# Optimization experiments

Measured on AMD Instinct MI355X. Metric: run time of the kernel, lower is better.

The kernel has to match this reference:

```python
import jax, jax.numpy as jnp
import numpy as np

B, N, E, H = 4, 4096, 1024, 16
D = E // H


def setup_inputs() -> dict:
    key = jax.random.key(0)
    ks = jax.random.split(key, 8)
    s = 1.0 / np.sqrt(E)
    x = jax.random.normal(ks[0], (B, N, E), dtype=jnp.float32)
    # binary multiplicative sparsity pattern over the head-head score matrix
    sparsity_pattern = jax.random.randint(ks[1], (H, H), 0, 2).astype(jnp.float32)
    Wq = jax.random.normal(ks[2], (E, E), dtype=jnp.float32) * s
    bq = jax.random.normal(ks[3], (E,), dtype=jnp.float32) * s
    Wk = jax.random.normal(ks[4], (E, E), dtype=jnp.float32) * s
    bk = jax.random.normal(ks[5], (E,), dtype=jnp.float32) * s
    Wv = jax.random.normal(ks[6], (E, E), dtype=jnp.float32) * s
    bv = jax.random.normal(ks[7], (E,), dtype=jnp.float32) * s
    return {"x": x, "sparsity_pattern": sparsity_pattern,
            "Wq": Wq, "bq": bq, "Wk": Wk, "bk": bk, "Wv": Wv, "bv": bv}


def reference(x, sparsity_pattern, Wq, bq, Wk, bk, Wv, bv):
    b, n, e = x.shape
    # torch Linear: y = x @ W.T + b
    q = (x @ Wq.T + bq).reshape(b, n, H, D)
    k = (x @ Wk.T + bk).reshape(b, n, H, D)
    v = (x @ Wv.T + bv).reshape(b, n, H, D)
    # torch.matmul over last two dims of [B,N,H,D]: scores are [B,N,H,H]
    scores = jnp.einsum('bnhd,bngd->bnhg', q, k) * sparsity_pattern
    attn = jax.nn.softmax(scores, axis=-1)
    out = jnp.einsum('bnhg,bngd->bnhd', attn, v).reshape(b, n, e)
    return out
```

## Files before the change

kernel.cpp:

```cpp
#include <hip/hip_runtime.h>
#include <hip/hip_bf16.h>

#define M_   16384
#define K_   1024
#define NQKV 3072

typedef _Float16 f16x4 __attribute__((ext_vector_type(4)));
typedef _Float16 f16x8 __attribute__((ext_vector_type(8)));
typedef float    f32x4 __attribute__((ext_vector_type(4)));

__global__ __launch_bounds__(256) void cvt_f32_f16(const float* __restrict__ in,
                                                   _Float16* __restrict__ o, int n4) {
  int i = blockIdx.x * blockDim.x + threadIdx.x;
  const int stride = gridDim.x * blockDim.x;
  for (; i < n4; i += stride) {
    float4 v = ((const float4*)in)[i];
    f16x4 h; h[0] = (_Float16)v.x; h[1] = (_Float16)v.y;
    h[2] = (_Float16)v.z; h[3] = (_Float16)v.w;
    *(f16x4*)&o[(size_t)i * 4] = h;
  }
}

__global__ __launch_bounds__(256) void cvt3_f32_f16(
    const float* __restrict__ a, const float* __restrict__ b,
    const float* __restrict__ c, _Float16* __restrict__ o, int n4each) {
  const float* src = (blockIdx.y == 0) ? a : (blockIdx.y == 1) ? b : c;
  _Float16* dst = o + (size_t)blockIdx.y * n4each * 4;
  int i = blockIdx.x * blockDim.x + threadIdx.x;
  const int stride = gridDim.x * blockDim.x;
  for (; i < n4each; i += stride) {
    float4 v = ((const float4*)src)[i];
    f16x4 h; h[0] = (_Float16)v.x; h[1] = (_Float16)v.y;
    h[2] = (_Float16)v.z; h[3] = (_Float16)v.w;
    *(f16x4*)&dst[(size_t)i * 4] = h;
  }
}

__global__ __launch_bounds__(512, 2) void gemm_qkv(
    const _Float16* __restrict__ xh, const _Float16* __restrict__ wh,
    const float* __restrict__ bq, const float* __restrict__ bk,
    const float* __restrict__ bv, _Float16* __restrict__ qkv)
{
  __shared__ __align__(16) _Float16 As[2][256 * 64];
  __shared__ __align__(16) _Float16 Bs[2][256 * 64];

  const int tid  = threadIdx.x;
  const int ln   = tid & 63;
  const int w    = tid >> 6;
  const int wm2  = w >> 2;
  const int wn4  = w & 3;
  const int lcol = ln & 15, quad = ln >> 4;

  const int bid = blockIdx.x;
  const int swz = (bid & 7) * 96 + (bid >> 3);
  const int m0 = (swz / 12) * 256;
  const int n0 = (swz % 12) * 256;

  f32x4 acc[8][4];
#pragma unroll
  for (int i = 0; i < 8; ++i)
#pragma unroll
    for (int j = 0; j < 4; ++j) acc[i][j] = f32x4{0.f, 0.f, 0.f, 0.f};

  f16x8 a0[4][2], a1[4][2], b0e[2][2], b0o[2][2], b1[2][2];

#define STAGE_A(BUF, KT, X)                                                    \
  { _Pragma("unroll")                                                          \
    for (int j = 0; j < 2; ++j) {                                              \
      const int c   = j * 512 + tid;                                           \
      const int rr  = c >> 3;                                                  \
      const int r   = (X) * 64 + (rr & 63) + ((rr >> 6) << 7);                 \
      const int cb  = (c & 7) ^ (r & 7);                                       \
      const int rr0 = j * 64 + w * 8;                                          \
      const int r0  = (X) * 64 + (rr0 & 63) + ((rr0 >> 6) << 7);               \
      __builtin_amdgcn_global_load_lds(                                        \
          (const __attribute__((address_space(1))) void*)(                     \
              xh + (size_t)(m0 + r) * K_ + (KT) * 64 + cb * 8),                \
          (__attribute__((address_space(3))) void*)(&As[BUF][r0 * 64]),        \
          16, 0, 0);                                                           \
    } }

#define STAGE_B(BUF, KT, Y)                                                    \
  { _Pragma("unroll")                                                          \
    for (int j = 0; j < 2; ++j) {                                              \
      const int c   = j * 512 + tid;                                           \
      const int rr  = c >> 3;                                                  \
      const int r   = ((rr >> 5) << 6) + (Y) * 32 + (rr & 31);                 \
      const int cb  = (c & 7) ^ (r & 7);                                       \
      const int rr0 = j * 64 + w * 8;                                          \
      const int r0  = ((rr0 >> 5) << 6) + (Y) * 32 + (rr0 & 31);               \
      __builtin_amdgcn_global_load_lds(                                        \
          (const __attribute__((address_space(1))) void*)(                     \
              wh + (size_t)(n0 + r) * K_ + (KT) * 64 + cb * 8),                \
          (__attribute__((address_space(3))) void*)(&Bs[BUF][r0 * 64]),        \
          16, 0, 0);                                                           \
    } }

#define RDA(DST, BUF, MH)                                                      \
  _Pragma("unroll")                                                            \
  for (int mi = 0; mi < 4; ++mi) {                                             \
    const int ar = wm2 * 128 + (MH) * 64 + mi * 16 + lcol;                     \
    const int sw = ar & 7;                                                     \
    DST[mi][0] = *(const f16x8*)&As[BUF][ar * 64 + ((quad    ) ^ sw) * 8];     \
    DST[mi][1] = *(const f16x8*)&As[BUF][ar * 64 + ((quad + 4) ^ sw) * 8];     \
  }

#define RDB(DST, BUF, NH)                                                      \
  _Pragma("unroll")                                                            \
  for (int ni = 0; ni < 2; ++ni) {                                             \
    const int br = wn4 * 64 + (NH) * 32 + ni * 16 + lcol;                      \
    const int sw = br & 7;                                                     \
    DST[ni][0] = *(const f16x8*)&Bs[BUF][br * 64 + ((quad    ) ^ sw) * 8];     \
    DST[ni][1] = *(const f16x8*)&Bs[BUF][br * 64 + ((quad + 4) ^ sw) * 8];     \
  }

#define MFMA16(AARR, BARR, MH, NH)                                             \
  __builtin_amdgcn_s_setprio(1);                                               \
  _Pragma("unroll")                                                            \
  for (int kb = 0; kb < 2; ++kb)                                               \
    _Pragma("unroll")                                                          \
    for (int mi = 0; mi < 4; ++mi)                                             \
      _Pragma("unroll")                                                        \
      for (int ni = 0; ni < 2; ++ni)                                           \
        acc[(MH) * 4 + mi][(NH) * 2 + ni] =                                    \
            __builtin_amdgcn_mfma_f32_16x16x32_f16(                            \
                AARR[mi][kb], BARR[ni][kb], acc[(MH) * 4 + mi][(NH) * 2 + ni], \
                0, 0, 0);                                                      \
  __builtin_amdgcn_s_setprio(0);

#define SB()    __builtin_amdgcn_sched_barrier(0)
#define BAR()   { __builtin_amdgcn_s_barrier(); SB(); }
#define LGKM(N) { asm volatile("s_waitcnt lgkmcnt(" #N ")" ::: "memory"); SB(); }
#define VM4()   { asm volatile("s_waitcnt vmcnt(4)" ::: "memory"); SB(); }
#define VM0()   { asm volatile("s_waitcnt vmcnt(0)" ::: "memory"); SB(); }

#define KTILE(CUR, B0C, B0N, T, NOTLAST)                                       \
  {                            \
    RDB(b1, CUR, 1); SB();                                                     \
    if (NOTLAST) {                                                             \
      STAGE_A(1 - (CUR), (T) + 1, 0); STAGE_B(1 - (CUR), (T) + 1, 0);          \
      STAGE_A(1 - (CUR), (T) + 1, 1); STAGE_B(1 - (CUR), (T) + 1, 1);          \
      SB();                                                                    \
    }                                                                          \
    LGKM(4);  MFMA16(a0, B0C, 0, 0);                                           \
    RDA(a1, CUR, 1); SB();                                                     \
    LGKM(8);  MFMA16(a0, b1, 0, 1);                                            \
    if (NOTLAST) VM4();                                                        \
    BAR();                                                                     \
        \
    if (NOTLAST) { RDA(a0, 1 - (CUR), 0); SB(); LGKM(8); }                     \
    else         { LGKM(0); }                                                  \
    MFMA16(a1, b1, 1, 1);                                                      \
    if (NOTLAST) { RDB(B0N, 1 - (CUR), 0); SB(); LGKM(4); }                    \
    else         { LGKM(0); }                                                  \
    MFMA16(a1, B0C, 1, 0);                                                     \
    if (NOTLAST) VM0();                                                        \
    BAR();                                                                     \
  }

  STAGE_A(0, 0, 0); STAGE_B(0, 0, 0); STAGE_A(0, 0, 1); STAGE_B(0, 0, 1);
  VM0(); BAR();
  RDA(a0, 0, 0); SB(); RDB(b0e, 0, 0); SB();

#pragma unroll 1
  for (int it = 0; it < 7; ++it) {
    KTILE(0, b0e, b0o, it * 2,     1);
    KTILE(1, b0o, b0e, it * 2 + 1, 1);
  }
  KTILE(0, b0e, b0o, 14, 1);
  KTILE(1, b0o, b0e, 15, 0);

#pragma unroll
  for (int nh = 0; nh < 4; ++nh) {
    const int col = n0 + wn4 * 64 + nh * 16 + lcol;
    const int seg = col >> 10, cs = col & 1023;
    const float bi = ((seg == 0) ? bq : (seg == 1) ? bk : bv)[cs];
#pragma unroll
    for (int mi = 0; mi < 8; ++mi) {
      const int r0 = m0 + wm2 * 128 + mi * 16 + quad * 4;
#pragma unroll
      for (int r = 0; r < 4; ++r)
        qkv[(size_t)(r0 + r) * 3072 + col] = (_Float16)(acc[mi][nh][r] + bi);
    }
  }
#undef STAGE_A
#undef STAGE_B
#undef RDA
#undef RDB
#undef MFMA16
#undef SB
#undef BAR
#undef LGKM
#undef VM4
#undef VM0
#undef KTILE
}

__global__ __launch_bounds__(256) void attn_kernel(
    const _Float16* __restrict__ qkv,
    const float* __restrict__ pat,
    float* __restrict__ out)
{
  __shared__ __align__(16) _Float16 Ps[4][16 * 24];
  __shared__ __align__(16) _Float16 Vt[4][64 * 24];

  const int tid  = threadIdx.x;
  const int ln   = tid & 63;
  const int wv   = tid >> 6;
  const int lcol = ln & 15, quad = ln >> 4;
  const int t    = blockIdx.x * 4 + wv;

  const _Float16* qg = qkv + (size_t)t * 3072;
  const _Float16* kg = qg + 1024;
  const _Float16* vg = qg + 2048;

  f16x8 vc[2];
  vc[0] = *(const f16x8*)(vg + ((ln >> 3)    ) * 64 + (ln & 7) * 8);
  vc[1] = *(const f16x8*)(vg + ((ln >> 3) + 8) * 64 + (ln & 7) * 8);
  f16x8 aq0 = *(const f16x8*)(qg + lcol * 64 + quad * 8);
  f16x8 aq1 = *(const f16x8*)(qg + lcol * 64 + 32 + quad * 8);
  f16x8 bk0 = *(const f16x8*)(kg + lcol * 64 + quad * 8);
  f16x8 bk1 = *(const f16x8*)(kg + lcol * 64 + 32 + quad * 8);
  float p4[4];
#pragma unroll
  for (int r = 0; r < 4; r++) p4[r] = pat[(quad * 4 + r) * 16 + lcol];

#pragma unroll
  for (int i = 0; i < 2; i++) {
    const int g = (ln >> 3) + i * 8, c = (ln & 7) * 8;
#pragma unroll
    for (int j = 0; j < 8; j++) Vt[wv][(c + j) * 24 + g] = vc[i][j];
  }

  f32x4 s = {0.f, 0.f, 0.f, 0.f};
  s = __builtin_amdgcn_mfma_f32_16x16x32_f16(aq0, bk0, s, 0, 0, 0);
  s = __builtin_amdgcn_mfma_f32_16x16x32_f16(aq1, bk1, s, 0, 0, 0);

#pragma unroll
  for (int r = 0; r < 4; r++) {
    const float sv = s[r] * p4[r];
    float m = sv;
#pragma unroll
    for (int msk = 1; msk < 16; msk <<= 1) m = fmaxf(m, __shfl_xor(m, msk, 64));
    const float e = __expf(sv - m);
    float su = e;
#pragma unroll
    for (int msk = 1; msk < 16; msk <<= 1) su += __shfl_xor(su, msk, 64);
    Ps[wv][(quad * 4 + r) * 24 + lcol] = (_Float16)(e / su);
  }

  f16x4 ap = *(const f16x4*)&Ps[wv][lcol * 24 + quad * 4];

  f32x4 o[4];
#pragma unroll
  for (int dt = 0; dt < 4; dt++) {
    f16x4 bvf = *(const f16x4*)&Vt[wv][(dt * 16 + lcol) * 24 + quad * 4];
    f32x4 z = {0.f, 0.f, 0.f, 0.f};
    o[dt] = __builtin_amdgcn_mfma_f32_16x16x16f16(ap, bvf, z, 0, 0, 0);
  }

  float* op = out + (size_t)t * 1024;
#pragma unroll
  for (int dt = 0; dt < 4; dt++)
#pragma unroll
    for (int r = 0; r < 4; r++)
      op[(quad * 4 + r) * 64 + dt * 16 + lcol] = o[dt][r];
}

extern "C" void kernel_launch(void* const* d_in, const int* in_sizes, int n_in,
                              void* d_out, int out_size, void* d_ws, size_t ws_size,
                              hipStream_t stream) {
  const float* x   = (const float*)d_in[0];
  const float* pat = (const float*)d_in[1];
  const float* Wq  = (const float*)d_in[2];
  const float* bq  = (const float*)d_in[3];
  const float* Wk  = (const float*)d_in[4];
  const float* bk  = (const float*)d_in[5];
  const float* Wv  = (const float*)d_in[6];
  const float* bv  = (const float*)d_in[7];

  _Float16* qkvh = (_Float16*)d_ws;
  _Float16* xh   = qkvh + (size_t)50331648;
  _Float16* wh   = qkvh + (size_t)67108864;

  cvt_f32_f16<<<4096, 256, 0, stream>>>(x, xh, 4194304);
  cvt3_f32_f16<<<dim3(256, 3), 256, 0, stream>>>(Wq, Wk, Wv, wh, 262144);

  gemm_qkv<<<768, 512, 0, stream>>>(xh, wh, bq, bk, bv, qkvh);
  attn_kernel<<<M_ / 4, 256, 0, stream>>>(qkvh, pat, (float*)d_out);
}
```

Before: 319.6 us.

## Restructure GEMM k-tile schedule with full LDS waits and single B0 buffer

Reorders the MFMA quadrants and LDS fragment reads inside each k-tile of the QKV projection GEMM. The ping-pong b0e/b0o registers become a single b0, and the fine-grained lgkmcnt/vmcnt(4) waits become full lgkmcnt(0)/vmcnt(0) waits. The aim is to cut register pressure and simplify the dependencies, but the coarser waits may expose LDS and global latency that the old schedule overlapped. The epilogue store loops of the GEMM and attention kernels are also reordered so each row's stores are grouped together.

Result: faster. 308.9 us (-3.3%).

```diff
diff --git a/kernel.cpp b/kernel.cpp
--- a/kernel.cpp
+++ b/kernel.cpp
@@ -62,7 +62,7 @@
 #pragma unroll
     for (int j = 0; j < 4; ++j) acc[i][j] = f32x4{0.f, 0.f, 0.f, 0.f};
 
-  f16x8 a0[4][2], a1[4][2], b0e[2][2], b0o[2][2], b1[2][2];
+  f16x8 a0[4][2], a1[4][2], b0[2][2], b1[2][2];
 
 #define STAGE_A(BUF, KT, X)                                                    \
   { _Pragma("unroll")                                                          \
@@ -130,57 +130,63 @@
 
 #define SB()    __builtin_amdgcn_sched_barrier(0)
 #define BAR()   { __builtin_amdgcn_s_barrier(); SB(); }
-#define LGKM(N) { asm volatile("s_waitcnt lgkmcnt(" #N ")" ::: "memory"); SB(); }
-#define VM4()   { asm volatile("s_waitcnt vmcnt(4)" ::: "memory"); SB(); }
+#define LGKM0() { asm volatile("s_waitcnt lgkmcnt(0)" ::: "memory"); SB(); }
 #define VM0()   { asm volatile("s_waitcnt vmcnt(0)" ::: "memory"); SB(); }
 
-#define KTILE(CUR, B0C, B0N, T, NOTLAST)                                       \
-  {                            \
+#define KTILE(CUR, T, NOTLAST)                                                 \
+  {                      \
+    RDA(a0, CUR, 0); SB();                                                     \
+    LGKM0();                       \
+                     \
     RDB(b1, CUR, 1); SB();                                                     \
     if (NOTLAST) {                                                             \
       STAGE_A(1 - (CUR), (T) + 1, 0); STAGE_B(1 - (CUR), (T) + 1, 0);          \
       STAGE_A(1 - (CUR), (T) + 1, 1); STAGE_B(1 - (CUR), (T) + 1, 1);          \
       SB();                                                                    \
     }                                                                          \
-    LGKM(4);  MFMA16(a0, B0C, 0, 0);                                           \
-    RDA(a1, CUR, 1); SB();                                                     \
-    LGKM(8);  MFMA16(a0, b1, 0, 1);                                            \
-    if (NOTLAST) VM4();                                                        \
-    BAR();                                                                     \
-        \
-    if (NOTLAST) { RDA(a0, 1 - (CUR), 0); SB(); LGKM(8); }                     \
-    else         { LGKM(0); }                                                  \
+    MFMA16(a0, b0, 0, 0);                                                      \
+                                            \
+    MFMA16(a1, b0, 1, 0);                                                      \
+    if (NOTLAST) VM0();                                                        \
+    BAR();                          \
+            \
+    LGKM0();                                                                   \
+    if (NOTLAST) { RDB(b0, 1 - (CUR), 0); SB(); }                              \
     MFMA16(a1, b1, 1, 1);                                                      \
-    if (NOTLAST) { RDB(B0N, 1 - (CUR), 0); SB(); LGKM(4); }                    \
-    else         { LGKM(0); }                                                  \
-    MFMA16(a1, B0C, 1, 0);                                                     \
-    if (NOTLAST) VM0();                                                        \
-    BAR();                                                                     \
+                                                  \
+    if (NOTLAST) { RDA(a1, 1 - (CUR), 1); SB(); }                              \
+    MFMA16(a0, b1, 0, 1);                                                      \
+    BAR();                                                           \
   }
 
   STAGE_A(0, 0, 0); STAGE_B(0, 0, 0); STAGE_A(0, 0, 1); STAGE_B(0, 0, 1);
   VM0(); BAR();
-  RDA(a0, 0, 0); SB(); RDB(b0e, 0, 0); SB();
+  RDB(b0, 0, 0); SB(); RDA(a1, 0, 1); SB();
 
 #pragma unroll 1
   for (int it = 0; it < 7; ++it) {
-    KTILE(0, b0e, b0o, it * 2,     1);
-    KTILE(1, b0o, b0e, it * 2 + 1, 1);
-  }
-  KTILE(0, b0e, b0o, 14, 1);
-  KTILE(1, b0o, b0e, 15, 0);
-
+    KTILE(0, it * 2,     1);
+    KTILE(1, it * 2 + 1, 1);
+  }
+  KTILE(0, 14, 1);
+  KTILE(1, 15, 0);
+
+  float bi4[4];
 #pragma unroll
   for (int nh = 0; nh < 4; ++nh) {
     const int col = n0 + wn4 * 64 + nh * 16 + lcol;
     const int seg = col >> 10, cs = col & 1023;
-    const float bi = ((seg == 0) ? bq : (seg == 1) ? bk : bv)[cs];
-#pragma unroll
-    for (int mi = 0; mi < 8; ++mi) {
-      const int r0 = m0 + wm2 * 128 + mi * 16 + quad * 4;
-#pragma unroll
-      for (int r = 0; r < 4; ++r)
-        qkv[(size_t)(r0 + r) * 3072 + col] = (_Float16)(acc[mi][nh][r] + bi);
+    bi4[nh] = ((seg == 0) ? bq : (seg == 1) ? bk : bv)[cs];
+  }
+#pragma unroll
+  for (int mi = 0; mi < 8; ++mi) {
+    const int r0 = m0 + wm2 * 128 + mi * 16 + quad * 4;
+#pragma unroll
+    for (int r = 0; r < 4; ++r) {
+      _Float16* rowp = qkv + (size_t)(r0 + r) * 3072 + n0 + wn4 * 64 + lcol;
+#pragma unroll
+      for (int nh = 0; nh < 4; ++nh)
+        rowp[nh * 16] = (_Float16)(acc[mi][nh][r] + bi4[nh]);
     }
   }
 #undef STAGE_A
@@ -190,8 +196,7 @@
 #undef MFMA16
 #undef SB
 #undef BAR
-#undef LGKM
-#undef VM4
+#undef LGKM0
 #undef VM0
 #undef KTILE
 }
@@ -261,10 +266,12 @@
 
   float* op = out + (size_t)t * 1024;
 #pragma unroll
-  for (int dt = 0; dt < 4; dt++)
-#pragma unroll
-    for (int r = 0; r < 4; r++)
-      op[(quad * 4 + r) * 64 + dt * 16 + lcol] = o[dt][r];
+  for (int r = 0; r < 4; r++) {
+    float* rp = op + (quad * 4 + r) * 64 + lcol;
+#pragma unroll
+    for (int dt = 0; dt < 4; dt++)
+      rp[dt * 16] = o[dt][r];
+  }
 }
 
 extern "C" void kernel_launch(void* const* d_in, const int* in_sizes, int n_in,
```
